# Kernel tuning notes

Hardware: AMD Instinct MI355X
Metric: run time of the kernel (lower is better)

## Reference

```python
import jax, jax.numpy as jnp
import numpy as np

N = 100000
E = 1600000
IN = 256
H = 4
F = 64
NEG_SLOPE = 0.05


def setup_inputs() -> dict:
    key = jax.random.key(0)
    ks = jax.random.split(key, 8)
    feat = jax.random.normal(ks[0], (N, IN), dtype=jnp.float32)
    src = jax.random.randint(ks[1], (E,), 0, N, dtype=jnp.int64)
    dst = jax.random.randint(ks[2], (E,), 0, N, dtype=jnp.int64)
    W_fc = jax.random.normal(ks[3], (H * F, IN), dtype=jnp.float32) * (2.0 / np.sqrt(IN + H * F))
    attn_l = jax.random.normal(ks[4], (H, F), dtype=jnp.float32) * 0.1
    attn_r = jax.random.normal(ks[5], (H, F), dtype=jnp.float32) * 0.1
    W_res = jax.random.normal(ks[6], (H * F, IN), dtype=jnp.float32) * (2.0 / np.sqrt(IN + H * F))
    bias = jnp.zeros((H * F,), dtype=jnp.float32)
    return {"feat": feat, "src": src, "dst": dst, "W_fc": W_fc,
            "attn_l": attn_l, "attn_r": attn_r, "W_res": W_res, "bias": bias}


def _leaky_relu(x):
    return jnp.where(x > 0, x, NEG_SLOPE * x)


def reference(feat, src, dst, W_fc, attn_l, attn_r, W_res, bias):
    # project: [N, H, F]
    feat_src = (feat @ W_fc.T).reshape(N, H, F)
    # attention logits per node: el/er [N, H]
    el = jnp.einsum('nhf,hf->nh', feat_src, attn_l)
    er = jnp.einsum('nhf,hf->nh', feat_src, attn_r)
    # edge SDDMM (u_add_v) + leaky_relu: [E, H]
    e = _leaky_relu(el[src] + er[dst])
    # edge softmax grouped by destination node
    emax = jax.ops.segment_max(e, dst, num_segments=N)          # [N, H]
    emax = jnp.where(jnp.isfinite(emax), emax, 0.0)             # empty segments
    ex = jnp.exp(e - emax[dst])                                 # [E, H]
    esum = jax.ops.segment_sum(ex, dst, num_segments=N)         # [N, H]
    a = ex / jnp.maximum(esum[dst], 1e-20)                      # [E, H]
    # u_mul_e + sum aggregation (SpMM): [N, H, F]
    msgs = feat_src[src] * a[:, :, None]                        # [E, H, F]
    rst = jax.ops.segment_sum(msgs, dst, num_segments=N)
    # residual + bias
    rst = rst + (feat @ W_res.T).reshape(N, H, F)
    rst = rst + bias.reshape(1, H, F)
    return rst, a
```

## Files before the change

kernel.cpp:

```cpp
#include <hip/hip_runtime.h>

#define NNODES 100000
#define NEDGES 1600000
#define KDIM 256
#define CDIM 256
#define NHEAD 4
#define FDIM 64
#define NEG 0.05f

typedef short bf16x8 __attribute__((ext_vector_type(8)));
typedef float f32x4  __attribute__((ext_vector_type(4)));
typedef __attribute__((address_space(3))) void*       lds_vp;
typedef __attribute__((address_space(1))) const void* glb_cvp;

__device__ __forceinline__ unsigned short f2b(float x) {
    unsigned int u = __float_as_uint(x);
    return (unsigned short)((u + 0x7FFFu + ((u >> 16) & 1u)) >> 16);
}
__device__ __forceinline__ float b2f(unsigned short b) {
    return __uint_as_float(((unsigned int)b) << 16);
}
__device__ __forceinline__ float lrelu(float x) { return x > 0.f ? x : NEG * x; }

__global__ __launch_bounds__(256) void cvt_feat(const float* __restrict__ in,
                                                unsigned short* __restrict__ out)
{
    int i = (blockIdx.x * 256 + threadIdx.x) * 4;
    float4 v = *(const float4*)(in + i);
    ushort4 o;
    o.x = f2b(v.x); o.y = f2b(v.y); o.z = f2b(v.z); o.w = f2b(v.w);
    *(ushort4*)(out + i) = o;
}

__global__ __launch_bounds__(256) void cvt_w(const float* __restrict__ Wfc,
                                             const float* __restrict__ Wres,
                                             unsigned short* __restrict__ out)
{
    int i = (blockIdx.x * 256 + threadIdx.x) * 4;
    float4 v = (i < 65536) ? *(const float4*)(Wfc + i)
                           : *(const float4*)(Wres + (i - 65536));
    ushort4 o;
    o.x = f2b(v.x); o.y = f2b(v.y); o.z = f2b(v.z); o.w = f2b(v.w);
    *(ushort4*)(out + i) = o;
}

__global__ __launch_bounds__(256) void gemm_mfma(
    const unsigned short* __restrict__ featb,
    const unsigned short* __restrict__ Wb,
    const float* __restrict__ bias,
    const float* __restrict__ attn_l, const float* __restrict__ attn_r,
    unsigned short* __restrict__ fsb,
    float* __restrict__ rst,
    float* __restrict__ el, float* __restrict__ er)
{
    const int b = blockIdx.x;
    const int grp = b >> 5, w32 = b & 31;
    const int bx = grp * 8 + (w32 & 7);
    const int ny = w32 >> 3;
    if (bx >= (NNODES + 127) / 128) return;

    __shared__ __align__(16) char smem[32768];
    char* sA = smem;
    char* sB = smem + 16384;

    const int tid = threadIdx.x;
    const int w = tid >> 6, l = tid & 63;
    const int wm = w & 1, wn = w >> 1;
    const int row0 = bx * 128;

    f32x4 acc[4][4];
#pragma unroll
    for (int tm = 0; tm < 4; ++tm)
#pragma unroll
        for (int tn = 0; tn < 4; ++tn) acc[tm][tn] = (f32x4)0.f;

    const int srow = tid >> 3;
    const int sslot = tid & 7;

    for (int k0 = 0; k0 < 256; k0 += 64) {
        if (k0) __syncthreads();
#pragma unroll
        for (int it = 0; it < 4; ++it) {
            int r = srow + it * 32;
            int gr = row0 + r; if (gr >= NNODES) gr = NNODES - 1;
            int kc = sslot ^ (r & 7);
            const unsigned short* g = featb + (size_t)gr * 256 + k0 + kc * 8;
            void* sp = sA + (it * 256 + w * 64) * 16;
            __builtin_amdgcn_global_load_lds((glb_cvp)g, (lds_vp)sp, 16, 0, 0);
        }
#pragma unroll
        for (int it = 0; it < 4; ++it) {
            int r = srow + it * 32;
            int kc = sslot ^ (r & 7);
            const unsigned short* g = Wb + (size_t)(ny * 128 + r) * 256 + k0 + kc * 8;
            void* sp = sB + (it * 256 + w * 64) * 16;
            __builtin_amdgcn_global_load_lds((glb_cvp)g, (lds_vp)sp, 16, 0, 0);
        }
        __syncthreads();

        const int quad = l >> 4;
#pragma unroll
        for (int kk = 0; kk < 2; ++kk) {
            const int kc = kk * 4 + quad;
            bf16x8 af[4], bq[4];
#pragma unroll
            for (int tm = 0; tm < 4; ++tm) {
                int m = wm * 64 + tm * 16 + (l & 15);
                af[tm] = *(const bf16x8*)(sA + m * 128 + ((kc ^ (m & 7)) * 16));
            }
#pragma unroll
            for (int tn = 0; tn < 4; ++tn) {
                int n = wn * 64 + tn * 16 + (l & 15);
                bq[tn] = *(const bf16x8*)(sB + n * 128 + ((kc ^ (n & 7)) * 16));
            }
#pragma unroll
            for (int tm = 0; tm < 4; ++tm)
#pragma unroll
                for (int tn = 0; tn < 4; ++tn)
                    acc[tm][tn] = __builtin_amdgcn_mfma_f32_16x16x32_bf16(
                        af[tm], bq[tn], acc[tm][tn], 0, 0, 0);
        }
    }

    const int quad = l >> 4, c15 = l & 15;
    if (ny < 2) {
#pragma unroll
        for (int tm = 0; tm < 4; ++tm) {
            int rb = row0 + wm * 64 + tm * 16 + quad * 4;
#pragma unroll
            for (int tn = 0; tn < 4; ++tn) {
                int cg = ny * 128 + wn * 64 + tn * 16 + c15;
#pragma unroll
                for (int reg = 0; reg < 4; ++reg) {
                    int r = rb + reg;
                    if (r < NNODES) fsb[(size_t)r * 256 + cg] = f2b(acc[tm][tn][reg]);
                }
            }
        }
        const int hh = ny * 2 + wn;
        float alv[4], arv[4];
#pragma unroll
        for (int tn = 0; tn < 4; ++tn) {
            alv[tn] = attn_l[hh * 64 + tn * 16 + c15];
            arv[tn] = attn_r[hh * 64 + tn * 16 + c15];
        }
#pragma unroll
        for (int tm = 0; tm < 4; ++tm) {
#pragma unroll
            for (int reg = 0; reg < 4; ++reg) {
                float pl = 0.f, pr = 0.f;
#pragma unroll
                for (int tn = 0; tn < 4; ++tn) {
                    float v = acc[tm][tn][reg];
                    pl = fmaf(v, alv[tn], pl);
                    pr = fmaf(v, arv[tn], pr);
                }
#pragma unroll
                for (int d = 1; d < 16; d <<= 1) {
                    pl += __shfl_xor(pl, d);
                    pr += __shfl_xor(pr, d);
                }
                if (c15 == 0) {
                    int r = row0 + wm * 64 + tm * 16 + quad * 4 + reg;
                    if (r < NNODES) {
                        el[r * NHEAD + hh] = pl;
                        er[r * NHEAD + hh] = pr;
                    }
                }
            }
        }
    } else {
#pragma unroll
        for (int tm = 0; tm < 4; ++tm) {
            int rb = row0 + wm * 64 + tm * 16 + quad * 4;
#pragma unroll
            for (int tn = 0; tn < 4; ++tn) {
                int co = (ny - 2) * 128 + wn * 64 + tn * 16 + c15;
                float b2 = bias[co];
#pragma unroll
                for (int reg = 0; reg < 4; ++reg) {
                    int r = rb + reg;
                    if (r < NNODES) rst[(size_t)r * 256 + co] = acc[tm][tn][reg] + b2;
                }
            }
        }
    }
}

__global__ __launch_bounds__(256) void count_kernel(const int* __restrict__ dst,
                                                    int* __restrict__ cnt)
{
    int e = blockIdx.x * 256 + threadIdx.x;
    if (e < NEDGES) atomicAdd(&cnt[dst[e]], 1);
}

__global__ __launch_bounds__(256) void offset_kernel(const int* __restrict__ cnt,
                                                     int* __restrict__ off,
                                                     int* __restrict__ cursor,
                                                     int* __restrict__ total)
{
    int n = blockIdx.x * 256 + threadIdx.x;
    int lane = threadIdx.x & 63;
    int c = (n < NNODES) ? cnt[n] : 0;
    int incl = c;
#pragma unroll
    for (int d = 1; d < 64; d <<= 1) {
        int t = __shfl_up(incl, d);
        if (lane >= d) incl += t;
    }
    int wsum = __shfl(incl, 63);
    int base = 0;
    if (lane == 0) base = atomicAdd(total, wsum);
    base = __shfl(base, 0);
    if (n < NNODES) {
        int o = base + incl - c;
        off[n] = o;
        cursor[n] = o;
    }
}

__global__ __launch_bounds__(256) void scatter_kernel(const int* __restrict__ dst,
                                                      int* __restrict__ cursor,
                                                      int* __restrict__ perm)
{
    int e = blockIdx.x * 256 + threadIdx.x;
    if (e < NEDGES) {
        int p = atomicAdd(&cursor[dst[e]], 1);
        perm[p] = e;
    }
}

__global__ __launch_bounds__(256) void agg_kernel(
    const int* __restrict__ src, const int* __restrict__ perm,
    const int* __restrict__ off, const int* __restrict__ cnt,
    const float* __restrict__ el, const float* __restrict__ er,
    const unsigned short* __restrict__ fsb,
    float* __restrict__ rst,
    float* __restrict__ a_out)
{
    const int tid = threadIdx.x;
    const int wv = tid >> 6, lane = tid & 63;
    const int n = blockIdx.x * 4 + wv;
    const int deg = cnt[n];
    if (deg == 0) return;
    const int o0 = off[n];
    const int h = lane >> 4;

    __shared__ __align__(16) float a_sh[4][64][4];
    float* aw = &a_sh[wv][0][0];

    const float4 er4 = *(const float4*)(er + (size_t)n * NHEAD);

    float4 m = make_float4(-1e30f, -1e30f, -1e30f, -1e30f);
    float4 s = make_float4(0.f, 0.f, 0.f, 0.f);
    int s0_save = 0, e0_save = 0; float4 l0_save = m;

    for (int base = 0; base < deg; base += 64) {
        int i = base + lane;
        bool valid = i < deg;
        int e = perm[o0 + (valid ? i : deg - 1)];
        int sidx = src[e];
        float4 ev = *(const float4*)(el + (size_t)sidx * NHEAD);
        float4 l;
        l.x = lrelu(ev.x + er4.x); l.y = lrelu(ev.y + er4.y);
        l.z = lrelu(ev.z + er4.z); l.w = lrelu(ev.w + er4.w);
        if (base == 0) { s0_save = sidx; e0_save = e; l0_save = l; }
        float mn;
        mn = fmaxf(m.x, l.x); s.x = s.x * __expf(m.x - mn) + (valid ? __expf(l.x - mn) : 0.f); m.x = mn;
        mn = fmaxf(m.y, l.y); s.y = s.y * __expf(m.y - mn) + (valid ? __expf(l.y - mn) : 0.f); m.y = mn;
        mn = fmaxf(m.z, l.z); s.z = s.z * __expf(m.z - mn) + (valid ? __expf(l.z - mn) : 0.f); m.z = mn;
        mn = fmaxf(m.w, l.w); s.w = s.w * __expf(m.w - mn) + (valid ? __expf(l.w - mn) : 0.f); m.w = mn;
    }
#pragma unroll
    for (int d = 32; d > 0; d >>= 1) {
        float mo, so, mn;
        mo = __shfl_xor(m.x, d); so = __shfl_xor(s.x, d);
        mn = fmaxf(m.x, mo); s.x = s.x * __expf(m.x - mn) + so * __expf(mo - mn); m.x = mn;
        mo = __shfl_xor(m.y, d); so = __shfl_xor(s.y, d);
        mn = fmaxf(m.y, mo); s.y = s.y * __expf(m.y - mn) + so * __expf(mo - mn); m.y = mn;
        mo = __shfl_xor(m.z, d); so = __shfl_xor(s.z, d);
        mn = fmaxf(m.z, mo); s.z = s.z * __expf(m.z - mn) + so * __expf(mo - mn); m.z = mn;
        mo = __shfl_xor(m.w, d); so = __shfl_xor(s.w, d);
        mn = fmaxf(m.w, mo); s.w = s.w * __expf(m.w - mn) + so * __expf(mo - mn); m.w = mn;
    }
    float4 inv;
    inv.x = 1.f / fmaxf(s.x, 1e-20f);
    inv.y = 1.f / fmaxf(s.y, 1e-20f);
    inv.z = 1.f / fmaxf(s.z, 1e-20f);
    inv.w = 1.f / fmaxf(s.w, 1e-20f);

    float4 acc = make_float4(0.f, 0.f, 0.f, 0.f);
    const int laneoff = lane << 2;
    for (int base = 0; base < deg; base += 64) {
        int i = base + lane;
        bool valid = i < deg;
        int sidx, e; float4 l;
        if (base == 0) { sidx = s0_save; e = e0_save; l = l0_save; }
        else {
            e = perm[o0 + (valid ? i : deg - 1)];
            sidx = src[e];
            float4 ev = *(const float4*)(el + (size_t)sidx * NHEAD);
            l.x = lrelu(ev.x + er4.x); l.y = lrelu(ev.y + er4.y);
            l.z = lrelu(ev.z + er4.z); l.w = lrelu(ev.w + er4.w);
        }
        float4 a;
        a.x = valid ? __expf(l.x - m.x) * inv.x : 0.f;
        a.y = valid ? __expf(l.y - m.y) * inv.y : 0.f;
        a.z = valid ? __expf(l.z - m.z) * inv.z : 0.f;
        a.w = valid ? __expf(l.w - m.w) * inv.w : 0.f;
        *(float4*)(aw + (lane << 2)) = a;

        if (valid) *(float4*)(a_out + (size_t)e * NHEAD) = a;

        int nc = min(64, deg - base);
#pragma unroll 8
        for (int j = 0; j < nc; ++j) {
            int sj = __builtin_amdgcn_readlane(sidx, j);
            float av = aw[(j << 2) + h];
            const unsigned short* rp = fsb + ((size_t)(unsigned)sj << 8) + laneoff;
            uint2 p = *(const uint2*)rp;
            acc.x = fmaf(av, __uint_as_float(p.x << 16), acc.x);
            acc.y = fmaf(av, __uint_as_float(p.x & 0xffff0000u), acc.y);
            acc.z = fmaf(av, __uint_as_float(p.y << 16), acc.z);
            acc.w = fmaf(av, __uint_as_float(p.y & 0xffff0000u), acc.w);
        }
    }
    size_t ro = (size_t)n * 256 + (lane << 2);
    float4 r = *(float4*)(rst + ro);
    r.x += acc.x; r.y += acc.y; r.z += acc.z; r.w += acc.w;
    *(float4*)(rst + ro) = r;
}

extern "C" void kernel_launch(void* const* d_in, const int* in_sizes, int n_in,
                              void* d_out, int out_size, void* d_ws, size_t ws_size,
                              hipStream_t stream) {
    const float* feat   = (const float*)d_in[0];
    const int*   src    = (const int*)d_in[1];
    const int*   dst    = (const int*)d_in[2];
    const float* Wfc    = (const float*)d_in[3];
    const float* attn_l = (const float*)d_in[4];
    const float* attn_r = (const float*)d_in[5];
    const float* Wres   = (const float*)d_in[6];
    const float* bias   = (const float*)d_in[7];

    float* rst   = (float*)d_out;
    float* a_out = (float*)d_out + (size_t)NNODES * CDIM;

    unsigned short* featb = (unsigned short*)d_ws;
    unsigned short* fsb   = featb + (size_t)NNODES * CDIM;
    unsigned short* Wb    = fsb + (size_t)NNODES * CDIM;
    float* el      = (float*)(Wb + 512 * 256);
    float* er      = el + (size_t)NNODES * NHEAD;
    int* cnt    = (int*)(er + (size_t)NNODES * NHEAD);
    int* off    = cnt + NNODES;
    int* cursor = off + NNODES;
    int* total  = cursor + NNODES;
    int* perm   = total + 4;

    hipMemsetAsync(cnt, 0, NNODES * sizeof(int), stream);
    hipMemsetAsync(total, 0, 4 * sizeof(int), stream);

    cvt_feat<<<(NNODES * CDIM) / (256 * 4), 256, 0, stream>>>(feat, featb);
    cvt_w<<<(512 * 256) / (256 * 4), 256, 0, stream>>>(Wfc, Wres, Wb);

    gemm_mfma<<<3136, 256, 0, stream>>>(featb, Wb, bias, attn_l, attn_r,
                                        fsb, rst, el, er);

    count_kernel<<<(NEDGES + 255) / 256, 256, 0, stream>>>(dst, cnt);
    offset_kernel<<<(NNODES + 255) / 256, 256, 0, stream>>>(cnt, off, cursor, total);
    scatter_kernel<<<(NEDGES + 255) / 256, 256, 0, stream>>>(dst, cursor, perm);

    agg_kernel<<<NNODES / 4, 256, 0, stream>>>(src, perm, off, cnt, el, er,
                                               fsb, rst, a_out);
}
```

Baseline: 674.8 us.

## Use global el max as softmax shift and gather two edges per wave step

Adds a small kernel that computes the per-head global maximum of el, so each node's softmax shift becomes lrelu(gmax+er), a fixed upper bound. This removes the online max/rescale exp work and the max merge in the wave reduction. The aggregation loop also changes so each half-wave handles a different edge with 16-byte loads, halving loop iterations at the cost of a final cross-half shuffle reduction. The fixed shift risks underflow when a node's logits sit far below the global max, and the new kernel adds a launch and a memset.

```diff
diff --git a/kernel.cpp b/kernel.cpp
--- a/kernel.cpp
+++ b/kernel.cpp
@@ -21,6 +21,14 @@
     return __uint_as_float(((unsigned int)b) << 16);
 }
 __device__ __forceinline__ float lrelu(float x) { return x > 0.f ? x : NEG * x; }
+
+__device__ __forceinline__ unsigned int fmap(float f) {
+    unsigned int u = __float_as_uint(f);
+    return u ^ ((u >> 31) ? 0xFFFFFFFFu : 0x80000000u);
+}
+__device__ __forceinline__ float funmap(unsigned int u) {
+    return __uint_as_float(u ^ ((u & 0x80000000u) ? 0x80000000u : 0xFFFFFFFFu));
+}
 
 __global__ __launch_bounds__(256) void cvt_feat(const float* __restrict__ in,
                                                 unsigned short* __restrict__ out)
@@ -187,6 +195,31 @@
     }
 }
 
+__global__ __launch_bounds__(256) void gmax_kernel(const float* __restrict__ el,
+                                                   unsigned int* __restrict__ gmax)
+{
+    int t = blockIdx.x * 256 + threadIdx.x;
+    float4 mx = make_float4(-1e30f, -1e30f, -1e30f, -1e30f);
+    for (int n = t; n < NNODES; n += 64 * 256) {
+        float4 v = *(const float4*)(el + (size_t)n * 4);
+        mx.x = fmaxf(mx.x, v.x); mx.y = fmaxf(mx.y, v.y);
+        mx.z = fmaxf(mx.z, v.z); mx.w = fmaxf(mx.w, v.w);
+    }
+#pragma unroll
+    for (int d = 32; d > 0; d >>= 1) {
+        mx.x = fmaxf(mx.x, __shfl_xor(mx.x, d));
+        mx.y = fmaxf(mx.y, __shfl_xor(mx.y, d));
+        mx.z = fmaxf(mx.z, __shfl_xor(mx.z, d));
+        mx.w = fmaxf(mx.w, __shfl_xor(mx.w, d));
+    }
+    if ((threadIdx.x & 63) == 0) {
+        atomicMax(&gmax[0], fmap(mx.x));
+        atomicMax(&gmax[1], fmap(mx.y));
+        atomicMax(&gmax[2], fmap(mx.z));
+        atomicMax(&gmax[3], fmap(mx.w));
+    }
+}
+
 __global__ __launch_bounds__(256) void count_kernel(const int* __restrict__ dst,
                                                     int* __restrict__ cnt)
 {
@@ -234,6 +267,7 @@
     const int* __restrict__ src, const int* __restrict__ perm,
     const int* __restrict__ off, const int* __restrict__ cnt,
     const float* __restrict__ el, const float* __restrict__ er,
+    const unsigned int* __restrict__ gmax,
     const unsigned short* __restrict__ fsb,
     float* __restrict__ rst,
     float* __restrict__ a_out)
@@ -244,16 +278,21 @@
     const int deg = cnt[n];
     if (deg == 0) return;
     const int o0 = off[n];
-    const int h = lane >> 4;
 
     __shared__ __align__(16) float a_sh[4][64][4];
     float* aw = &a_sh[wv][0][0];
 
     const float4 er4 = *(const float4*)(er + (size_t)n * NHEAD);
-
-    float4 m = make_float4(-1e30f, -1e30f, -1e30f, -1e30f);
+    const uint4 g4 = *(const uint4*)gmax;
+    float4 M;
+    M.x = lrelu(funmap(g4.x) + er4.x);
+    M.y = lrelu(funmap(g4.y) + er4.y);
+    M.z = lrelu(funmap(g4.z) + er4.z);
+    M.w = lrelu(funmap(g4.w) + er4.w);
+
     float4 s = make_float4(0.f, 0.f, 0.f, 0.f);
-    int s0_save = 0, e0_save = 0; float4 l0_save = m;
+    int s0_save = 0, e0_save = 0;
+    float4 l0_save = make_float4(0.f, 0.f, 0.f, 0.f);
 
     for (int base = 0; base < deg; base += 64) {
         int i = base + lane;
@@ -265,23 +304,17 @@
         l.x = lrelu(ev.x + er4.x); l.y = lrelu(ev.y + er4.y);
         l.z = lrelu(ev.z + er4.z); l.w = lrelu(ev.w + er4.w);
         if (base == 0) { s0_save = sidx; e0_save = e; l0_save = l; }
-        float mn;
-        mn = fmaxf(m.x, l.x); s.x = s.x * __expf(m.x - mn) + (valid ? __expf(l.x - mn) : 0.f); m.x = mn;
-        mn = fmaxf(m.y, l.y); s.y = s.y * __expf(m.y - mn) + (valid ? __expf(l.y - mn) : 0.f); m.y = mn;
-        mn = fmaxf(m.z, l.z); s.z = s.z * __expf(m.z - mn) + (valid ? __expf(l.z - mn) : 0.f); m.z = mn;
-        mn = fmaxf(m.w, l.w); s.w = s.w * __expf(m.w - mn) + (valid ? __expf(l.w - mn) : 0.f); m.w = mn;
+        s.x += valid ? __expf(l.x - M.x) : 0.f;
+        s.y += valid ? __expf(l.y - M.y) : 0.f;
+        s.z += valid ? __expf(l.z - M.z) : 0.f;
+        s.w += valid ? __expf(l.w - M.w) : 0.f;
     }
 #pragma unroll
     for (int d = 32; d > 0; d >>= 1) {
-        float mo, so, mn;
-        mo = __shfl_xor(m.x, d); so = __shfl_xor(s.x, d);
-        mn = fmaxf(m.x, mo); s.x = s.x * __expf(m.x - mn) + so * __expf(mo - mn); m.x = mn;
-        mo = __shfl_xor(m.y, d); so = __shfl_xor(s.y, d);
-        mn = fmaxf(m.y, mo); s.y = s.y * __expf(m.y - mn) + so * __expf(mo - mn); m.y = mn;
-        mo = __shfl_xor(m.z, d); so = __shfl_xor(s.z, d);
-        mn = fmaxf(m.z, mo); s.z = s.z * __expf(m.z - mn) + so * __expf(mo - mn); m.z = mn;
-        mo = __shfl_xor(m.w, d); so = __shfl_xor(s.w, d);
-        mn = fmaxf(m.w, mo); s.w = s.w * __expf(m.w - mn) + so * __expf(mo - mn); m.w = mn;
+        s.x += __shfl_xor(s.x, d);
+        s.y += __shfl_xor(s.y, d);
+        s.z += __shfl_xor(s.z, d);
+        s.w += __shfl_xor(s.w, d);
     }
     float4 inv;
     inv.x = 1.f / fmaxf(s.x, 1e-20f);
@@ -289,8 +322,15 @@
     inv.z = 1.f / fmaxf(s.z, 1e-20f);
     inv.w = 1.f / fmaxf(s.w, 1e-20f);
 
-    float4 acc = make_float4(0.f, 0.f, 0.f, 0.f);
-    const int laneoff = lane << 2;
+    const int rsel = lane >> 5;
+    const int c    = lane & 31;
+    const int h2   = c >> 3;
+    const unsigned int coff = (unsigned)c << 4;
+
+    float acc[8];
+#pragma unroll
+    for (int k = 0; k < 8; ++k) acc[k] = 0.f;
+
     for (int base = 0; base < deg; base += 64) {
         int i = base + lane;
         bool valid = i < deg;
@@ -304,30 +344,42 @@
             l.z = lrelu(ev.z + er4.z); l.w = lrelu(ev.w + er4.w);
         }
         float4 a;
-        a.x = valid ? __expf(l.x - m.x) * inv.x : 0.f;
-        a.y = valid ? __expf(l.y - m.y) * inv.y : 0.f;
-        a.z = valid ? __expf(l.z - m.z) * inv.z : 0.f;
-        a.w = valid ? __expf(l.w - m.w) * inv.w : 0.f;
+        a.x = valid ? __expf(l.x - M.x) * inv.x : 0.f;
+        a.y = valid ? __expf(l.y - M.y) * inv.y : 0.f;
+        a.z = valid ? __expf(l.z - M.z) * inv.z : 0.f;
+        a.w = valid ? __expf(l.w - M.w) * inv.w : 0.f;
         *(float4*)(aw + (lane << 2)) = a;
 
         if (valid) *(float4*)(a_out + (size_t)e * NHEAD) = a;
 
         int nc = min(64, deg - base);
-#pragma unroll 8
-        for (int j = 0; j < nc; ++j) {
-            int sj = __builtin_amdgcn_readlane(sidx, j);
-            float av = aw[(j << 2) + h];
-            const unsigned short* rp = fsb + ((size_t)(unsigned)sj << 8) + laneoff;
-            uint2 p = *(const uint2*)rp;
-            acc.x = fmaf(av, __uint_as_float(p.x << 16), acc.x);
-            acc.y = fmaf(av, __uint_as_float(p.x & 0xffff0000u), acc.y);
-            acc.z = fmaf(av, __uint_as_float(p.y << 16), acc.z);
-            acc.w = fmaf(av, __uint_as_float(p.y & 0xffff0000u), acc.w);
-        }
-    }
-    size_t ro = (size_t)n * 256 + (lane << 2);
+#pragma unroll 4
+        for (int jj = 0; jj < nc; jj += 2) {
+            int sjA = __builtin_amdgcn_readlane(sidx, jj);
+            int sjB = __builtin_amdgcn_readlane(sidx, jj + 1);
+            float av = aw[((jj + rsel) << 2) + h2];
+            int sj = rsel ? sjB : sjA;
+            unsigned int boff = ((unsigned)sj << 9) + coff;
+            uint4 p = *(const uint4*)((const char*)fsb + boff);
+            acc[0] = fmaf(av, __uint_as_float(p.x << 16),         acc[0]);
+            acc[1] = fmaf(av, __uint_as_float(p.x & 0xffff0000u), acc[1]);
+            acc[2] = fmaf(av, __uint_as_float(p.y << 16),         acc[2]);
+            acc[3] = fmaf(av, __uint_as_float(p.y & 0xffff0000u), acc[3]);
+            acc[4] = fmaf(av, __uint_as_float(p.z << 16),         acc[4]);
+            acc[5] = fmaf(av, __uint_as_float(p.z & 0xffff0000u), acc[5]);
+            acc[6] = fmaf(av, __uint_as_float(p.w << 16),         acc[6]);
+            acc[7] = fmaf(av, __uint_as_float(p.w & 0xffff0000u), acc[7]);
+        }
+    }
+#pragma unroll
+    for (int k = 0; k < 8; ++k) acc[k] += __shfl_xor(acc[k], 32);
+    float o0v = rsel ? acc[4] : acc[0];
+    float o1v = rsel ? acc[5] : acc[1];
+    float o2v = rsel ? acc[6] : acc[2];
+    float o3v = rsel ? acc[7] : acc[3];
+    size_t ro = (size_t)n * 256 + ((size_t)c << 3) + ((size_t)rsel << 2);
     float4 r = *(float4*)(rst + ro);
-    r.x += acc.x; r.y += acc.y; r.z += acc.z; r.w += acc.w;
+    r.x += o0v; r.y += o1v; r.z += o2v; r.w += o3v;
     *(float4*)(rst + ro) = r;
 }
 
@@ -351,7 +403,8 @@
     unsigned short* Wb    = fsb + (size_t)NNODES * CDIM;
     float* el      = (float*)(Wb + 512 * 256);
     float* er      = el + (size_t)NNODES * NHEAD;
-    int* cnt    = (int*)(er + (size_t)NNODES * NHEAD);
+    unsigned int* gmax = (unsigned int*)(er + (size_t)NNODES * NHEAD);
+    int* cnt    = (int*)(gmax + 4);
     int* off    = cnt + NNODES;
     int* cursor = off + NNODES;
     int* total  = cursor + NNODES;
@@ -359,17 +412,20 @@
 
     hipMemsetAsync(cnt, 0, NNODES * sizeof(int), stream);
     hipMemsetAsync(total, 0, 4 * sizeof(int), stream);
+    hipMemsetAsync(gmax, 0, 4 * sizeof(unsigned int), stream);
 
     cvt_feat<<<(NNODES * CDIM) / (256 * 4), 256, 0, stream>>>(feat, featb);
     cvt_w<<<(512 * 256) / (256 * 4), 256, 0, stream>>>(Wfc, Wres, Wb);
 
     gemm_mfma<<<3136, 256, 0, stream>>>(featb, Wb, bias, attn_l, attn_r,
                                         fsb, rst, el, er);
+
+    gmax_kernel<<<64, 256, 0, stream>>>(el, gmax);
 
     count_kernel<<<(NEDGES + 255) / 256, 256, 0, stream>>>(dst, cnt);
     offset_kernel<<<(NNODES + 255) / 256, 256, 0, stream>>>(cnt, off, cursor, total);
     scatter_kernel<<<(NEDGES + 255) / 256, 256, 0, stream>>>(dst, cursor, perm);
 
-    agg_kernel<<<NNODES / 4, 256, 0, stream>>>(src, perm, off, cnt, el, er,
+    agg_kernel<<<NNODES / 4, 256, 0, stream>>>(src, perm, off, cnt, el, er, gmax,
                                                fsb, rst, a_out);
 }
```

After: 691.6 us. 1.02x slower.
